# Kernel optimization log

Hardware: AMD Instinct MI355X
Metric: run time of the kernel (lower is better)

The kernel has to match this reference:

```python
import jax, jax.numpy as jnp
import numpy as np

_IDENTITY = jnp.array([1, 0, 0, 0], dtype=jnp.float32)

G, T, P, B = 512, 128, 256, 512  # num_graphs, max_terms, n_params, batch


def setup_inputs() -> dict:
    key = jax.random.key(0)
    k0, k1, k2, k3, k4 = jax.random.split(key, 5)
    psi_const = jax.random.randint(k0, (G, T), 0, 2).astype(jnp.int32)
    psi_params = jax.random.randint(k1, (G, T, P), 0, 2).astype(jnp.float32)
    phi_const = jax.random.randint(k2, (G, T), 0, 2).astype(jnp.int32)
    phi_params = jax.random.randint(k3, (G, T, P), 0, 2).astype(jnp.float32)
    param_vals = jax.random.randint(k4, (B, P), 0, 2).astype(jnp.float32)
    return {
        "psi_const": psi_const,
        "psi_params": psi_params,
        "phi_const": phi_const,
        "phi_params": phi_params,
        "param_vals": param_vals,
    }


def reference(psi_const, psi_params, phi_const, phi_params, param_vals):
    # GF(2) matmul: contract bitmasks with binary parameter values, mod 2.
    # psi_params: (G,T,P), param_vals: (B,P) -> (B,G,T)
    psi = jnp.mod(psi_const[None].astype(jnp.float32)
                  + jnp.einsum("gtp,bp->bgt", psi_params, param_vals), 2.0)
    phi = jnp.mod(phi_const[None].astype(jnp.float32)
                  + jnp.einsum("gtp,bp->bgt", phi_params, param_vals), 2.0)
    # Elementwise parity product and mod-2 sum over terms -> (B,G)
    exponent = jnp.mod(psi * phi, 2.0)
    sum_exponents = jnp.mod(jnp.sum(exponent, axis=-1), 2.0)
    # Parity-to-sign: (-1)^e = 1 - 2e, embedded as exact scalar (B,G,4)
    summands_exact = (1.0 - 2.0 * sum_exponents)[..., None] * _IDENTITY
    return summands_exact
```

## Files before the change

kernel.cpp:

```cpp
#include <hip/hip_runtime.h>

typedef unsigned long long u64;

#define G 512
#define T 128
#define P 256
#define B 512

#define PV_OFF    0
#define PAR_OFF   16384
#define WS_NEEDED (PAR_OFF + (size_t)G * 16 * 4)


__device__ __forceinline__ unsigned nzbit(unsigned u) {
    return (u | (0u - u)) >> 31;
}

__device__ __forceinline__ u64 pack64(const uint4* sv) {
    uint4 f[16];
    #pragma unroll
    for (int i = 0; i < 16; ++i) f[i] = sv[i];
    __builtin_amdgcn_sched_barrier(0);
    unsigned lo = 0, hi = 0;
    #pragma unroll
    for (int i = 0; i < 8; ++i) {
        lo |= nzbit(f[i].x) << (4 * i + 0);
        lo |= nzbit(f[i].y) << (4 * i + 1);
        lo |= nzbit(f[i].z) << (4 * i + 2);
        lo |= nzbit(f[i].w) << (4 * i + 3);
    }
    #pragma unroll
    for (int i = 8; i < 16; ++i) {
        hi |= nzbit(f[i].x) << (4 * (i - 8) + 0);
        hi |= nzbit(f[i].y) << (4 * (i - 8) + 1);
        hi |= nzbit(f[i].z) << (4 * (i - 8) + 2);
        hi |= nzbit(f[i].w) << (4 * (i - 8) + 3);
    }
    return ((u64)hi << 32) | (u64)lo;
}

__global__ __launch_bounds__(256) void pack_pv_zero_kernel(
    const float* __restrict__ pv, u64* __restrict__ pv_ws,
    uint4* __restrict__ par_zero)
{
    int tid = blockIdx.x * 256 + threadIdx.x;
    pv_ws[tid] = pack64((const uint4*)(pv + (size_t)tid * 64));
    par_zero[tid] = make_uint4(0, 0, 0, 0);
}

#define LSTR 9

__global__ __launch_bounds__(256, 6) void pi_half_kernel(
    const int*   __restrict__ psi_const,
    const int*   __restrict__ phi_const,
    const float* __restrict__ psi_params,
    const float* __restrict__ phi_params,
    const u64*   __restrict__ pv,
    unsigned*    __restrict__ par_ws)
{
    __shared__ u64 lds[64 * LSTR];

    const int g    = blockIdx.x >> 1;
    const int half = blockIdx.x & 1;
    const int tid  = threadIdx.x;
    const int lane = tid & 63;
    const int wv   = tid >> 6;

    const size_t rowbase = ((size_t)g * T + half * 64) * P;

    #pragma unroll
    for (int rep = 0; rep < 2; ++rep) {
        int w    = rep * 256 + tid;
        int t    = w >> 3;
        int slot = w & 7;
        const float* s = (slot < 4 ? psi_params : phi_params)
                         + rowbase + (size_t)t * P + (slot & 3) * 64;
        lds[t * LSTR + slot] = pack64((const uint4*)s);
    }
    __syncthreads();

    u64 ra[8];
    #pragma unroll
    for (int k = 0; k < 8; ++k) ra[k] = lds[lane * LSTR + k];

    const int tg = g * T + half * 64 + lane;
    unsigned pa = ((unsigned)psi_const[tg]) & 1u;
    unsigned qa = ((unsigned)phi_const[tg]) & 1u;

    unsigned a0, a1, a2, a3;
    #pragma unroll
    for (int q = 0; q < 4; ++q) {
        int b0  = wv * 128 + q * 32;
        int b0u = __builtin_amdgcn_readfirstlane(b0);
        const u64* vp = pv + (size_t)b0u * 4;

        unsigned acc = 0;
        #pragma unroll
        for (int i = 0; i < 32; ++i) {
            u64 v0 = vp[i * 4 + 0], v1 = vp[i * 4 + 1];
            u64 v2 = vp[i * 4 + 2], v3 = vp[i * 4 + 3];
            u64 m0 = (ra[0] & v0) ^ (ra[1] & v1) ^ (ra[2] & v2) ^ (ra[3] & v3);
            u64 m1 = (ra[4] & v0) ^ (ra[5] & v1) ^ (ra[6] & v2) ^ (ra[7] & v3);
            unsigned f0 = (unsigned)m0 ^ (unsigned)(m0 >> 32);
            unsigned f1 = (unsigned)m1 ^ (unsigned)(m1 >> 32);
            unsigned t01 = ((unsigned)__popc(f0) ^ pa) & ((unsigned)__popc(f1) ^ qa);
            acc ^= (t01 & 1u) << i;
        }
        if (q == 0) a0 = acc; else if (q == 1) a1 = acc;
        else if (q == 2) a2 = acc; else a3 = acc;
    }

    #pragma unroll
    for (int m = 1; m < 64; m <<= 1) {
        a0 ^= __shfl_xor(a0, m, 64);
        a1 ^= __shfl_xor(a1, m, 64);
        a2 ^= __shfl_xor(a2, m, 64);
        a3 ^= __shfl_xor(a3, m, 64);
    }
    if (lane < 4) {
        unsigned myv = (lane == 0) ? a0 : (lane == 1) ? a1 : (lane == 2) ? a2 : a3;
        atomicXor(&par_ws[g * 16 + wv * 4 + lane], myv);
    }
}

__global__ __launch_bounds__(256) void epilogue_kernel(
    const unsigned* __restrict__ par_ws, float4* __restrict__ out)
{
    int id = blockIdx.x * 256 + threadIdx.x;
    int b  = id >> 9;
    int gg = id & 511;
    unsigned w = par_ws[gg * 16 + (b >> 5)];
    float s = 1.0f - 2.0f * (float)((w >> (b & 31)) & 1u);
    out[id] = make_float4(s, 0.0f, 0.0f, 0.0f);
}

struct __align__(16) U64x2 { u64 x, y; };

__global__ __launch_bounds__(256) void pack_pv_kernel(
    const float* __restrict__ pv, u64* __restrict__ out)
{
    int lane = threadIdx.x & 63;
    int wave = threadIdx.x >> 6;
    int row  = blockIdx.x * 4 + wave;
    const float4* src = (const float4*)(pv + (size_t)row * P);
    float4 f = src[lane];
    u64 w0 = __ballot(f.x != 0.0f);
    u64 w1 = __ballot(f.y != 0.0f);
    u64 w2 = __ballot(f.z != 0.0f);
    u64 w3 = __ballot(f.w != 0.0f);
    if (lane == 0) {
        out[row * 4 + 0] = w0;
        out[row * 4 + 1] = w1;
        out[row * 4 + 2] = w2;
        out[row * 4 + 3] = w3;
    }
}

__global__ __launch_bounds__(512) void pi_main_kernel(
    const int*   __restrict__ psi_const,
    const float* __restrict__ psi_params,
    const int*   __restrict__ phi_const,
    const float* __restrict__ phi_params,
    const u64*   __restrict__ pv,
    float4*      __restrict__ out)
{
    __shared__ __align__(16) u64 rows[T * 8];
    __shared__ unsigned code_sm[T];

    const int g    = blockIdx.x;
    const int tid  = threadIdx.x;
    const int lane = tid & 63;
    const int wave = tid >> 6;

    if (tid < T) {
        unsigned pc = ((unsigned)psi_const[g * T + tid]) & 1u;
        unsigned qc = ((unsigned)phi_const[g * T + tid]) & 1u;
        code_sm[tid] = pc | (qc << 1);
    }

    for (int i = 0; i < 32; ++i) {
        int r = wave * 32 + i;
        int t = r & (T - 1);
        const float* mat = (r < T) ? psi_params : phi_params;
        int off = (r < T) ? 0 : 4;
        const float4* src = (const float4*)(mat + ((size_t)g * T + t) * P);
        float4 f = src[lane];
        u64 w0 = __ballot(f.x != 0.0f);
        u64 w1 = __ballot(f.y != 0.0f);
        u64 w2 = __ballot(f.z != 0.0f);
        u64 w3 = __ballot(f.w != 0.0f);
        if (lane == 0) {
            U64x2* d = (U64x2*)&rows[t * 8 + off];
            U64x2 a; a.x = w0; a.y = w1;
            U64x2 c; c.x = w2; c.y = w3;
            d[0] = a;
            d[1] = c;
        }
    }
    __syncthreads();

    const int b = tid;
    const u64* v = pv + (size_t)b * 4;
    u64 v0 = v[0], v1 = v[1], v2 = v[2], v3 = v[3];

    unsigned e = 0;
    #pragma unroll 8
    for (int t = 0; t < T; ++t) {
        const U64x2* row = (const U64x2*)&rows[t * 8];
        U64x2 p0 = row[0], p1 = row[1], q0 = row[2], q1 = row[3];
        u64 ma = (p0.x & v0) ^ (p0.y & v1) ^ (p1.x & v2) ^ (p1.y & v3);
        u64 mb = (q0.x & v0) ^ (q0.y & v1) ^ (q1.x & v2) ^ (q1.y & v3);
        unsigned c = code_sm[t];
        e ^= (((unsigned)__popcll(ma) ^ c) & ((unsigned)__popcll(mb) ^ (c >> 1)));
    }
    e &= 1u;

    float s = 1.0f - 2.0f * (float)e;
    out[(size_t)b * G + g] = make_float4(s, 0.0f, 0.0f, 0.0f);
}

extern "C" void kernel_launch(void* const* d_in, const int* in_sizes, int n_in,
                              void* d_out, int out_size, void* d_ws, size_t ws_size,
                              hipStream_t stream) {
    const int*   psi_const  = (const int*)  d_in[0];
    const float* psi_params = (const float*)d_in[1];
    const int*   phi_const  = (const int*)  d_in[2];
    const float* phi_params = (const float*)d_in[3];
    const float* param_vals = (const float*)d_in[4];

    if (ws_size >= WS_NEEDED) {
        u64*      pv_ws  = (u64*)((char*)d_ws + PV_OFF);
        unsigned* par_ws = (unsigned*)((char*)d_ws + PAR_OFF);

        pack_pv_zero_kernel<<<8, 256, 0, stream>>>(
            param_vals, pv_ws, (uint4*)par_ws);
        pi_half_kernel<<<G * 2, 256, 0, stream>>>(
            psi_const, phi_const, psi_params, phi_params, pv_ws, par_ws);
        epilogue_kernel<<<(B * G) / 256, 256, 0, stream>>>(
            par_ws, (float4*)d_out);
    } else {
        u64* pv_packed = (u64*)d_ws;
        pack_pv_kernel<<<B / 4, 256, 0, stream>>>(param_vals, pv_packed);
        pi_main_kernel<<<G, 512, 0, stream>>>(psi_const, psi_params,
                                              phi_const, phi_params,
                                              pv_packed, (float4*)d_out);
    }
}
```

Measured before the change: 185.1 us.

## Split main kernel into single-wave blocks over 4-term groups with LDS DMA staging

Replaces the half-graph 256-thread kernel with 16384 single-wave blocks, each handling 4 terms of one graph. The param rows are staged into LDS with global_load_lds and packed via ballot. Each lane then owns one batch element per chunk and reduces parity with a ballot instead of shuffle trees. The aim is more parallelism and lower per-block latency and register pressure. The cost is many more atomicXor operations on par_ws and more blocks to launch.

```diff
diff --git a/kernel.cpp b/kernel.cpp
--- a/kernel.cpp
+++ b/kernel.cpp
@@ -1,6 +1,7 @@
 #include <hip/hip_runtime.h>
 
 typedef unsigned long long u64;
+typedef unsigned int u32;
 
 #define G 512
 #define T 128
@@ -48,79 +49,87 @@
     par_zero[tid] = make_uint4(0, 0, 0, 0);
 }
 
-#define LSTR 9
-
-__global__ __launch_bounds__(256, 6) void pi_half_kernel(
+#define GRP 4
+#define NGRP (T / GRP)
+#define MAIN_BLOCKS (G * NGRP)
+
+__global__ __launch_bounds__(64, 4) void pi_group_kernel(
     const int*   __restrict__ psi_const,
     const int*   __restrict__ phi_const,
     const float* __restrict__ psi_params,
     const float* __restrict__ phi_params,
-    const u64*   __restrict__ pv,
+    const u64*   __restrict__ pv_ws,
     unsigned*    __restrict__ par_ws)
 {
-    __shared__ u64 lds[64 * LSTR];
-
-    const int g    = blockIdx.x >> 1;
-    const int half = blockIdx.x & 1;
-    const int tid  = threadIdx.x;
-    const int lane = tid & 63;
-    const int wv   = tid >> 6;
-
-    const size_t rowbase = ((size_t)g * T + half * 64) * P;
-
-    #pragma unroll
-    for (int rep = 0; rep < 2; ++rep) {
-        int w    = rep * 256 + tid;
-        int t    = w >> 3;
-        int slot = w & 7;
-        const float* s = (slot < 4 ? psi_params : phi_params)
-                         + rowbase + (size_t)t * P + (slot & 3) * 64;
-        lds[t * LSTR + slot] = pack64((const uint4*)s);
-    }
-    __syncthreads();
-
-    u64 ra[8];
-    #pragma unroll
-    for (int k = 0; k < 8; ++k) ra[k] = lds[lane * LSTR + k];
-
-    const int tg = g * T + half * 64 + lane;
-    unsigned pa = ((unsigned)psi_const[tg]) & 1u;
-    unsigned qa = ((unsigned)phi_const[tg]) & 1u;
-
-    unsigned a0, a1, a2, a3;
-    #pragma unroll
-    for (int q = 0; q < 4; ++q) {
-        int b0  = wv * 128 + q * 32;
-        int b0u = __builtin_amdgcn_readfirstlane(b0);
-        const u64* vp = pv + (size_t)b0u * 4;
-
-        unsigned acc = 0;
+    __shared__ __align__(16) float stage[2 * GRP * 256];
+
+    const int lane = threadIdx.x;
+    const int g    = blockIdx.x >> 5;
+    const int grp  = blockIdx.x & (NGRP - 1);
+
+    const float* ps = psi_params + ((size_t)g * T + grp * GRP) * P;
+    const float* qs = phi_params + ((size_t)g * T + grp * GRP) * P;
+
+    #pragma unroll
+    for (int k = 0; k < 4; ++k) {
+        __builtin_amdgcn_global_load_lds(
+            (const __attribute__((address_space(1))) u32*)(ps + k * 256 + lane * 4),
+            (__attribute__((address_space(3))) u32*)&stage[k * 256],
+            16, 0, 0);
+    }
+    #pragma unroll
+    for (int k = 0; k < 4; ++k) {
+        __builtin_amdgcn_global_load_lds(
+            (const __attribute__((address_space(1))) u32*)(qs + k * 256 + lane * 4),
+            (__attribute__((address_space(3))) u32*)&stage[1024 + k * 256],
+            16, 0, 0);
+    }
+    asm volatile("s_waitcnt vmcnt(0)" ::: "memory");
+
+    u64 ra[GRP][8];
+    #pragma unroll
+    for (int t = 0; t < GRP; ++t) {
         #pragma unroll
-        for (int i = 0; i < 32; ++i) {
-            u64 v0 = vp[i * 4 + 0], v1 = vp[i * 4 + 1];
-            u64 v2 = vp[i * 4 + 2], v3 = vp[i * 4 + 3];
-            u64 m0 = (ra[0] & v0) ^ (ra[1] & v1) ^ (ra[2] & v2) ^ (ra[3] & v3);
-            u64 m1 = (ra[4] & v0) ^ (ra[5] & v1) ^ (ra[6] & v2) ^ (ra[7] & v3);
-            unsigned f0 = (unsigned)m0 ^ (unsigned)(m0 >> 32);
-            unsigned f1 = (unsigned)m1 ^ (unsigned)(m1 >> 32);
-            unsigned t01 = ((unsigned)__popc(f0) ^ pa) & ((unsigned)__popc(f1) ^ qa);
-            acc ^= (t01 & 1u) << i;
+        for (int j = 0; j < 4; ++j) {
+            float xp = stage[t * 256 + j * 64 + lane];
+            ra[t][j]     = __ballot(xp != 0.0f);
+            float xq = stage[1024 + t * 256 + j * 64 + lane];
+            ra[t][4 + j] = __ballot(xq != 0.0f);
         }
-        if (q == 0) a0 = acc; else if (q == 1) a1 = acc;
-        else if (q == 2) a2 = acc; else a3 = acc;
-    }
-
-    #pragma unroll
-    for (int m = 1; m < 64; m <<= 1) {
-        a0 ^= __shfl_xor(a0, m, 64);
-        a1 ^= __shfl_xor(a1, m, 64);
-        a2 ^= __shfl_xor(a2, m, 64);
-        a3 ^= __shfl_xor(a3, m, 64);
-    }
-    if (lane < 4) {
-        unsigned myv = (lane == 0) ? a0 : (lane == 1) ? a1 : (lane == 2) ? a2 : a3;
-        atomicXor(&par_ws[g * 16 + wv * 4 + lane], myv);
-    }
+    }
+
+    unsigned pa[GRP], qa[GRP];
+    #pragma unroll
+    for (int t = 0; t < GRP; ++t) {
+        pa[t] = ((unsigned)psi_const[g * T + grp * GRP + t]) & 1u;
+        qa[t] = ((unsigned)phi_const[g * T + grp * GRP + t]) & 1u;
+    }
+
+    unsigned wacc = 0;
+    #pragma unroll
+    for (int c = 0; c < 8; ++c) {
+        const ulonglong2* vp =
+            (const ulonglong2*)(pv_ws + ((size_t)(c * 64) + lane) * 4);
+        ulonglong2 ua = vp[0], ub = vp[1];
+        u64 v0 = ua.x, v1 = ua.y, v2 = ub.x, v3 = ub.y;
+
+        unsigned e = 0;
+        #pragma unroll
+        for (int t = 0; t < GRP; ++t) {
+            u64 m0 = (ra[t][0] & v0) ^ (ra[t][1] & v1)
+                   ^ (ra[t][2] & v2) ^ (ra[t][3] & v3);
+            u64 m1 = (ra[t][4] & v0) ^ (ra[t][5] & v1)
+                   ^ (ra[t][6] & v2) ^ (ra[t][7] & v3);
+            e ^= (((unsigned)__popcll(m0) ^ pa[t])
+                & ((unsigned)__popcll(m1) ^ qa[t]));
+        }
+
+        u64 bal = __ballot(e & 1u);
+        if (lane == 2 * c)     wacc = (unsigned)bal;
+        if (lane == 2 * c + 1) wacc = (unsigned)(bal >> 32);
+    }
+
+    if (lane < 16) atomicXor(&par_ws[g * 16 + lane], wacc);
 }
 
 __global__ __launch_bounds__(256) void epilogue_kernel(
@@ -234,7 +243,7 @@
 
         pack_pv_zero_kernel<<<8, 256, 0, stream>>>(
             param_vals, pv_ws, (uint4*)par_ws);
-        pi_half_kernel<<<G * 2, 256, 0, stream>>>(
+        pi_group_kernel<<<MAIN_BLOCKS, 64, 0, stream>>>(
             psi_const, phi_const, psi_params, phi_params, pv_ws, par_ws);
         epilogue_kernel<<<(B * G) / 256, 256, 0, stream>>>(
             par_ws, (float4*)d_out);
```

New measurement: 172.0 us. 1.08x faster.
